# Kernel tuning notes

Measured on AMD Instinct MI355X. Metric: run time of the kernel, lower is better.

The kernel has to match this reference:

```python
import jax, jax.numpy as jnp
import numpy as np


def setup_inputs() -> dict:
    key = jax.random.key(0)
    ks = jax.random.split(key, 7)
    B, S, D, E, R, K = 64, 577, 1024, 8, 16, 2
    x = jax.random.normal(ks[0], (B, S, D), dtype=jnp.float32)
    top_k_indices = jax.random.randint(ks[1], (B, K), 0, E, dtype=jnp.int64)
    # gates are softmax over top-k logits in the original GatingNetwork
    top_k_gates = jax.nn.softmax(jax.random.normal(ks[2], (B, K), dtype=jnp.float32), axis=-1)
    weight_fixed = jax.random.normal(ks[3], (D, D), dtype=jnp.float32) * 0.02
    A_all = jax.random.normal(ks[4], (E, R, D), dtype=jnp.float32) * 0.02
    B_all = jax.random.normal(ks[5], (E, D, R), dtype=jnp.float32) * 0.02
    bias = jax.random.normal(ks[6], (D,), dtype=jnp.float32) * 0.02
    return {"x": x, "top_k_indices": top_k_indices, "top_k_gates": top_k_gates,
            "weight_fixed": weight_fixed, "A_all": A_all, "B_all": B_all, "bias": bias}


def reference(x, top_k_indices, top_k_gates, weight_fixed, A_all, B_all, bias):
    # x: [B,S,D]; top_k_indices/gates: [B,K]; weight_fixed: [O,D]
    # A_all: [E,R,D]; B_all: [E,O,R]; bias: [O]
    output_fixed = jnp.einsum('bsd,od->bso', x, weight_fixed)
    A_sel = A_all[top_k_indices]            # [B,K,R,D] gathered per-batch expert A
    B_sel = B_all[top_k_indices]            # [B,K,O,R]
    x_a = jnp.einsum('bsd,bkrd->bksr', x, A_sel)          # x @ A^T per chosen expert
    expert_out = jnp.einsum('bksr,bkor->bkso', x_a, B_sel)  # (xA^T) @ B^T
    expert_output = jnp.einsum('bkso,bk->bso', expert_out, top_k_gates)
    return output_fixed + expert_output + bias
```

## Files before the change

### kernel.cpp

```cpp
#include <hip/hip_runtime.h>
#include <hip/hip_bf16.h>
#include <stdint.h>

#define M_REAL 36928LL
#define M_PAD  36992LL
#define DDIM   1024
#define SSEQ   577
#define NBATCH 64

typedef __attribute__((ext_vector_type(8))) short bf16x8;
typedef __attribute__((ext_vector_type(4))) float f32x4;

#define XBF_OFF   0ULL
#define WBF_OFF   75759616ULL
#define ABF_OFF   77856768ULL
#define XABF_OFF  78118912ULL
#define GBBF_OFF  80486400ULL
#define WS_NEED   84680704ULL

__device__ __forceinline__ unsigned short f2bf(float f) {
  union { float f; unsigned int u; } v; v.f = f;
  unsigned int u = v.u;
  unsigned int r = (u + 0x7fffu + ((u >> 16) & 1u)) >> 16;
  return (unsigned short)r;
}

__device__ __forceinline__ bf16x8 cvt8(const float* __restrict__ p) {
  float4 a = *(const float4*)p;
  float4 b = *(const float4*)(p + 4);
  bf16x8 o;
  o[0] = (short)f2bf(a.x); o[1] = (short)f2bf(a.y);
  o[2] = (short)f2bf(a.z); o[3] = (short)f2bf(a.w);
  o[4] = (short)f2bf(b.x); o[5] = (short)f2bf(b.y);
  o[6] = (short)f2bf(b.z); o[7] = (short)f2bf(b.w);
  return o;
}

#define GLOAD_LDS16(gsrc, ldst)                                                  \
  __builtin_amdgcn_global_load_lds((const __attribute__((address_space(1))) void*)(gsrc), \
                                   (__attribute__((address_space(3))) void*)(ldst), 16, 0, 0)

__global__ void prep_kernel(const float* __restrict__ W,
                            const float* __restrict__ A_all,
                            const float* __restrict__ B_all,
                            const int* __restrict__ idx,
                            const float* __restrict__ gates,
                            unsigned short* __restrict__ wbf,
                            unsigned short* __restrict__ abf,
                            unsigned short* __restrict__ gbbf,
                            unsigned short* __restrict__ xbf,
                            unsigned short* __restrict__ xabf) {
  const int W_UNITS = 131072;
  const int A_UNITS = 16384;
  const int G_UNITS = 65536;
  const int XP_UNITS = 8192;
  const int P_UNITS = 2048;
  const int TOTAL = W_UNITS + A_UNITS + G_UNITS + XP_UNITS + P_UNITS;
  int u = blockIdx.x * blockDim.x + threadIdx.x;
  int stride = gridDim.x * blockDim.x;
  for (; u < TOTAL; u += stride) {
    if (u < W_UNITS) {
      int i = u * 8;
      *(bf16x8*)(wbf + i) = cvt8(W + i);
    } else if (u < W_UNITS + A_UNITS) {
      int i = (u - W_UNITS) * 8;
      *(bf16x8*)(abf + i) = cvt8(A_all + i);
    } else if (u < W_UNITS + A_UNITS + G_UNITS) {
      int v = u - W_UNITS - A_UNITS;
      int b = v >> 10;
      int n = v & 1023;
      unsigned short tmp[32];
#pragma unroll
      for (int k = 0; k < 2; ++k) {
        int e = idx[b * 2 + k];
        float g = gates[b * 2 + k];
        const float* Br = B_all + ((size_t)e * 1024 + n) * 16;
#pragma unroll
        for (int r = 0; r < 16; ++r) tmp[k * 16 + r] = f2bf(g * Br[r]);
      }
      unsigned short* dst = gbbf + (size_t)v * 32;
#pragma unroll
      for (int j = 0; j < 32; ++j) dst[j] = tmp[j];
    } else if (u < W_UNITS + A_UNITS + G_UNITS + XP_UNITS) {
      int v = u - W_UNITS - A_UNITS - G_UNITS;
      bf16x8 z;
#pragma unroll
      for (int j = 0; j < 8; ++j) z[j] = 0;
      *(bf16x8*)(xbf + (size_t)M_REAL * DDIM + (size_t)v * 8) = z;
    } else {
      int v = u - W_UNITS - A_UNITS - G_UNITS - XP_UNITS;
      xabf[(size_t)M_REAL * 32 + v] = 0;
    }
  }
}

__global__ __launch_bounds__(256) void cast_xa_kernel(
    const float* __restrict__ x,
    const unsigned short* __restrict__ abf,
    const int* __restrict__ idx,
    unsigned short* __restrict__ xbf,
    unsigned short* __restrict__ xabf) {
  int bid = blockIdx.x;
  int b = bid / 10;
  int s0 = (bid % 10) * 64;
  int wave = threadIdx.x >> 6;
  int lane = threadIdx.x & 63;
  int l15 = lane & 15, lhi = lane >> 4;

  int srow = s0 + wave * 16 + l15;
  bool valid = srow < SSEQ;
  long long mrow = (long long)b * SSEQ + (valid ? srow : 0);
  const float* xrow = x + (size_t)mrow * DDIM;
  unsigned short* xbrow = xbf + (size_t)mrow * DDIM;
  int e0 = idx[b * 2 + 0], e1 = idx[b * 2 + 1];
  const unsigned short* ar0 = abf + ((size_t)e0 * 16 + l15) * DDIM;
  const unsigned short* ar1 = abf + ((size_t)e1 * 16 + l15) * DDIM;

  f32x4 acc0 = {0.f, 0.f, 0.f, 0.f}, acc1 = {0.f, 0.f, 0.f, 0.f};
  for (int k = 0; k < DDIM; k += 32) {
    int ko = k + lhi * 8;
    bf16x8 a;
    if (valid) {
      a = cvt8(xrow + ko);
      *(bf16x8*)(xbrow + ko) = a;
    } else {
#pragma unroll
      for (int j = 0; j < 8; ++j) a[j] = 0;
    }
    bf16x8 b0 = *(const bf16x8*)(ar0 + ko);
    bf16x8 b1 = *(const bf16x8*)(ar1 + ko);
    acc0 = __builtin_amdgcn_mfma_f32_16x16x32_bf16(a, b0, acc0, 0, 0, 0);
    acc1 = __builtin_amdgcn_mfma_f32_16x16x32_bf16(a, b1, acc1, 0, 0, 0);
  }
  int sout = s0 + wave * 16 + lhi * 4;
#pragma unroll
  for (int reg = 0; reg < 4; ++reg) {
    int s = sout + reg;
    if (s < SSEQ) {
      size_t mo = ((size_t)b * SSEQ + s) * 32;
      xabf[mo + l15]      = f2bf(acc0[reg]);
      xabf[mo + 16 + l15] = f2bf(acc1[reg]);
    }
  }
}

#define BM 128
#define BN 128
#define BKT 64
__global__ __launch_bounds__(256, 2) void gemm_kernel(
    const unsigned short* __restrict__ xbf,
    const unsigned short* __restrict__ wbf,
    const unsigned short* __restrict__ xabf,
    const unsigned short* __restrict__ gbbf,
    const float* __restrict__ bias,
    float* __restrict__ out) {
  __shared__ unsigned short As0[8192], As1[8192];
  __shared__ unsigned short Bs0[8192], Bs1[8192];

  int g = blockIdx.x;
  int xcd = g & 7, gi = g >> 3;
  int wg = xcd * 289 + gi;
  const int bm = wg >> 3;
  const int bn = wg & 7;
  const long long m0 = (long long)bm * BM;
  const int n0 = bn * BN;

  const int tid = threadIdx.x;
  const int wave = tid >> 6, lane = tid & 63;
  const int l15 = lane & 15, lhi = lane >> 4;
  const int wm = (wave >> 1) * 64, wn = (wave & 1) * 64;

  f32x4 acc[4][4];
#pragma unroll
  for (int i = 0; i < 4; ++i)
#pragma unroll
    for (int j = 0; j < 4; ++j) acc[i][j] = (f32x4){0.f, 0.f, 0.f, 0.f};

  const int rowbase = wave * 32;
  const int rl = lane >> 3;
  const int csrc = (((lane & 7) ^ rl) << 3);

  const int sl0 = ((lhi ^ (l15 & 7)) << 3);
  const int sl1 = sl0 ^ 32;

#define STAGE(t, As_, Bs_)                                                       \
  do { const size_t ko = (size_t)(t) * BKT;                                      \
    _Pragma("unroll")                                                            \
    for (int i = 0; i < 4; ++i) {                                                \
      int r = rowbase + i * 8;                                                   \
      GLOAD_LDS16(xbf + (size_t)(m0 + r + rl) * DDIM + ko + csrc, &As_[r * BKT]);\
    }                                                                            \
    _Pragma("unroll")                                                            \
    for (int i = 0; i < 4; ++i) {                                                \
      int r = rowbase + i * 8;                                                   \
      GLOAD_LDS16(wbf + (size_t)(n0 + r + rl) * DDIM + ko + csrc, &Bs_[r * BKT]);\
    } } while (0)

#define COMPUTE(As_, Bs_)                                                        \
  do { bf16x8 af[4][2], bfv[4][2];                                               \
    _Pragma("unroll")                                                            \
    for (int f = 0; f < 4; ++f) {                                                \
      af[f][0]  = *(const bf16x8*)&As_[(wm + f * 16 + l15) * BKT + sl0];         \
      af[f][1]  = *(const bf16x8*)&As_[(wm + f * 16 + l15) * BKT + sl1];         \
      bfv[f][0] = *(const bf16x8*)&Bs_[(wn + f * 16 + l15) * BKT + sl0];         \
      bfv[f][1] = *(const bf16x8*)&Bs_[(wn + f * 16 + l15) * BKT + sl1];         \
    }                                                                            \
    _Pragma("unroll")                                                            \
    for (int i = 0; i < 4; ++i)                                                  \
      _Pragma("unroll")                                                          \
      for (int j = 0; j < 4; ++j)                                                \
        _Pragma("unroll")                                                        \
        for (int ks = 0; ks < 2; ++ks)                                           \
          acc[i][j] = __builtin_amdgcn_mfma_f32_16x16x32_bf16(                   \
              af[i][ks], bfv[j][ks], acc[i][j], 0, 0, 0);                        \
  } while (0)

#define BAR() do { __builtin_amdgcn_s_barrier(); asm volatile("" ::: "memory"); } while (0)
#define LGKM0() asm volatile("s_waitcnt lgkmcnt(0)" ::: "memory")
#define VM8() asm volatile("s_waitcnt vmcnt(8)" ::: "memory")
#define VM0() asm volatile("s_waitcnt vmcnt(0)" ::: "memory")

  STAGE(0, As0, Bs0);
  STAGE(1, As1, Bs1);
  VM8();
  BAR();

#pragma unroll 1
  for (int i = 0; i < 8; ++i) {
    const int t = 2 * i;
    COMPUTE(As0, Bs0);
    LGKM0(); BAR();
    if (t + 2 < 16) { STAGE(t + 2, As0, Bs0); VM8(); }
    else            { VM0(); }
    BAR();
    COMPUTE(As1, Bs1);
    if (t + 3 < 16) {
      LGKM0(); BAR();
      STAGE(t + 3, As1, Bs1); VM8();
      BAR();
    }
  }
#undef STAGE
#undef COMPUTE

  long long mlast = m0 + BM - 1; if (mlast > M_REAL - 1) mlast = M_REAL - 1;
  int b_lo = (int)(m0 / SSEQ);
  int b_hi = (int)(mlast / SSEQ);
  for (int bs = b_lo; bs <= b_hi; ++bs) {
    bf16x8 af[4], bfv[4];
#pragma unroll
    for (int f = 0; f < 4; ++f) {
      long long m = m0 + wm + f * 16 + l15;
      bf16x8 v = *(const bf16x8*)&xabf[(size_t)m * 32 + lhi * 8];
      if ((int)(m / SSEQ) != bs) {
#pragma unroll
        for (int j = 0; j < 8; ++j) v[j] = 0;
      }
      af[f] = v;
      int n = n0 + wn + f * 16 + l15;
      bfv[f] = *(const bf16x8*)&gbbf[((size_t)bs * 1024 + n) * 32 + lhi * 8];
    }
#pragma unroll
    for (int i = 0; i < 4; ++i)
#pragma unroll
      for (int j = 0; j < 4; ++j)
        acc[i][j] = __builtin_amdgcn_mfma_f32_16x16x32_bf16(af[i], bfv[j], acc[i][j], 0, 0, 0);
  }

  {
    float* lfs = (float*)(wave < 2 ? (void*)As0 : (void*)Bs0);
    const int ebase = (wave & 1) * 1104;
    const long long mrow0 = m0 + wm;
    const int ncol0 = n0 + wn;
#pragma unroll
    for (int i = 0; i < 4; ++i) {
#pragma unroll
      for (int j = 0; j < 4; ++j) {
        float bv = bias[ncol0 + j * 16 + l15];
#pragma unroll
        for (int reg = 0; reg < 4; ++reg)
          lfs[ebase + (lhi * 4 + reg) * 68 + j * 16 + l15] = acc[i][j][reg] + bv;
      }
#pragma unroll
      for (int rr = 0; rr < 4; ++rr) {
        int row = rr * 4 + lhi;
        f32x4 v = *(const f32x4*)&lfs[ebase + row * 68 + l15 * 4];
        long long m = mrow0 + i * 16 + row;
        if (m < M_REAL)
          __builtin_nontemporal_store(v, (f32x4*)&out[m * DDIM + ncol0 + l15 * 4]);
      }
    }
  }
}

extern "C" void kernel_launch(void* const* d_in, const int* in_sizes, int n_in,
                              void* d_out, int out_size, void* d_ws, size_t ws_size,
                              hipStream_t stream) {
  const float* x      = (const float*)d_in[0];
  const int*   idx    = (const int*)d_in[1];
  const float* gates  = (const float*)d_in[2];
  const float* W      = (const float*)d_in[3];
  const float* A_all  = (const float*)d_in[4];
  const float* B_all  = (const float*)d_in[5];
  const float* bias   = (const float*)d_in[6];
  float* out = (float*)d_out;

  char* ws = (char*)d_ws;
  unsigned short* xbf  = (unsigned short*)(ws + XBF_OFF);
  unsigned short* wbf  = (unsigned short*)(ws + WBF_OFF);
  unsigned short* abf  = (unsigned short*)(ws + ABF_OFF);
  unsigned short* xabf = (unsigned short*)(ws + XABF_OFF);
  unsigned short* gbbf = (unsigned short*)(ws + GBBF_OFF);

  prep_kernel<<<dim3(872), dim3(256), 0, stream>>>(W, A_all, B_all, idx, gates,
                                                   wbf, abf, gbbf, xbf, xabf);
  cast_xa_kernel<<<dim3(640), dim3(256), 0, stream>>>(x, abf, idx, xbf, xabf);
  gemm_kernel<<<dim3(2312), dim3(256), 0, stream>>>(xbf, wbf, xabf, gbbf, bias, out);
}
```

Baseline: 153.2 us.

## Load weight operand fragments directly from global into registers, bypassing LDS

Removes the shared-memory staging buffers for the weight tile and has each wave read its B fragments straight from global memory into registers one k-step ahead. The A tile is still double-buffered in LDS, and the wait counts are adjusted to the new load mix. This halves LDS use and removes the B LDS writes and reads. In exchange, B global loads are narrow, strided and duplicated across waves, and their latency is only partly hidden by a single step of prefetch.

Measured after the change: 241.5 us. 1.58x slower.

```diff
diff --git a/kernel.cpp b/kernel.cpp
--- a/kernel.cpp
+++ b/kernel.cpp
@@ -155,7 +155,6 @@
     const float* __restrict__ bias,
     float* __restrict__ out) {
   __shared__ unsigned short As0[8192], As1[8192];
-  __shared__ unsigned short Bs0[8192], Bs1[8192];
 
   int g = blockIdx.x;
   int xcd = g & 7, gi = g >> 3;
@@ -183,27 +182,31 @@
   const int sl0 = ((lhi ^ (l15 & 7)) << 3);
   const int sl1 = sl0 ^ 32;
 
-#define STAGE(t, As_, Bs_)                                                       \
+  const unsigned short* bpB = wbf + (size_t)(n0 + wn + l15) * DDIM + lhi * 8;
+  bf16x8 bfv[4][2];
+
+#define STAGE_A(t, As_)                                                          \
   do { const size_t ko = (size_t)(t) * BKT;                                      \
     _Pragma("unroll")                                                            \
     for (int i = 0; i < 4; ++i) {                                                \
       int r = rowbase + i * 8;                                                   \
       GLOAD_LDS16(xbf + (size_t)(m0 + r + rl) * DDIM + ko + csrc, &As_[r * BKT]);\
-    }                                                                            \
-    _Pragma("unroll")                                                            \
-    for (int i = 0; i < 4; ++i) {                                                \
-      int r = rowbase + i * 8;                                                   \
-      GLOAD_LDS16(wbf + (size_t)(n0 + r + rl) * DDIM + ko + csrc, &Bs_[r * BKT]);\
     } } while (0)
 
-#define COMPUTE(As_, Bs_)                                                        \
-  do { bf16x8 af[4][2], bfv[4][2];                                               \
+#define LOADB(t)                                                                 \
+  do { const size_t ko = (size_t)(t) * BKT;                                      \
     _Pragma("unroll")                                                            \
     for (int f = 0; f < 4; ++f) {                                                \
-      af[f][0]  = *(const bf16x8*)&As_[(wm + f * 16 + l15) * BKT + sl0];         \
-      af[f][1]  = *(const bf16x8*)&As_[(wm + f * 16 + l15) * BKT + sl1];         \
-      bfv[f][0] = *(const bf16x8*)&Bs_[(wn + f * 16 + l15) * BKT + sl0];         \
-      bfv[f][1] = *(const bf16x8*)&Bs_[(wn + f * 16 + l15) * BKT + sl1];         \
+      bfv[f][0] = *(const bf16x8*)(bpB + (size_t)f * 16 * DDIM + ko);            \
+      bfv[f][1] = *(const bf16x8*)(bpB + (size_t)f * 16 * DDIM + ko + 32);       \
+    } } while (0)
+
+#define COMPUTE(As_)                                                             \
+  do { bf16x8 af[4][2];                                                          \
+    _Pragma("unroll")                                                            \
+    for (int f = 0; f < 4; ++f) {                                                \
+      af[f][0] = *(const bf16x8*)&As_[(wm + f * 16 + l15) * BKT + sl0];          \
+      af[f][1] = *(const bf16x8*)&As_[(wm + f * 16 + l15) * BKT + sl1];          \
     }                                                                            \
     _Pragma("unroll")                                                            \
     for (int i = 0; i < 4; ++i)                                                  \
@@ -217,37 +220,41 @@
 
 #define BAR() do { __builtin_amdgcn_s_barrier(); asm volatile("" ::: "memory"); } while (0)
 #define LGKM0() asm volatile("s_waitcnt lgkmcnt(0)" ::: "memory")
-#define VM8() asm volatile("s_waitcnt vmcnt(8)" ::: "memory")
+#define VM4() asm volatile("s_waitcnt vmcnt(4)" ::: "memory")
 #define VM0() asm volatile("s_waitcnt vmcnt(0)" ::: "memory")
 
-  STAGE(0, As0, Bs0);
-  STAGE(1, As1, Bs1);
-  VM8();
+  STAGE_A(0, As0);
+  LOADB(0);
+  STAGE_A(1, As1);
+  VM4();
   BAR();
 
 #pragma unroll 1
   for (int i = 0; i < 8; ++i) {
     const int t = 2 * i;
-    COMPUTE(As0, Bs0);
+    COMPUTE(As0);
     LGKM0(); BAR();
-    if (t + 2 < 16) { STAGE(t + 2, As0, Bs0); VM8(); }
+    LOADB(t + 1);
+    if (t + 2 < 16) { STAGE_A(t + 2, As0); VM4(); }
     else            { VM0(); }
     BAR();
-    COMPUTE(As1, Bs1);
+    COMPUTE(As1);
     if (t + 3 < 16) {
       LGKM0(); BAR();
-      STAGE(t + 3, As1, Bs1); VM8();
+      LOADB(t + 2);
+      STAGE_A(t + 3, As1); VM4();
       BAR();
     }
   }
-#undef STAGE
+#undef STAGE_A
+#undef LOADB
 #undef COMPUTE
 
   long long mlast = m0 + BM - 1; if (mlast > M_REAL - 1) mlast = M_REAL - 1;
   int b_lo = (int)(m0 / SSEQ);
   int b_hi = (int)(mlast / SSEQ);
   for (int bs = b_lo; bs <= b_hi; ++bs) {
-    bf16x8 af[4], bfv[4];
+    bf16x8 af[4], bfw[4];
 #pragma unroll
     for (int f = 0; f < 4; ++f) {
       long long m = m0 + wm + f * 16 + l15;
@@ -258,17 +265,19 @@
       }
       af[f] = v;
       int n = n0 + wn + f * 16 + l15;
-      bfv[f] = *(const bf16x8*)&gbbf[((size_t)bs * 1024 + n) * 32 + lhi * 8];
+      bfw[f] = *(const bf16x8*)&gbbf[((size_t)bs * 1024 + n) * 32 + lhi * 8];
     }
 #pragma unroll
     for (int i = 0; i < 4; ++i)
 #pragma unroll
       for (int j = 0; j < 4; ++j)
-        acc[i][j] = __builtin_amdgcn_mfma_f32_16x16x32_bf16(af[i], bfv[j], acc[i][j], 0, 0, 0);
-  }
+        acc[i][j] = __builtin_amdgcn_mfma_f32_16x16x32_bf16(af[i], bfw[j], acc[i][j], 0, 0, 0);
+  }
+
+  LGKM0(); BAR();
 
   {
-    float* lfs = (float*)(wave < 2 ? (void*)As0 : (void*)Bs0);
+    float* lfs = (float*)(wave < 2 ? (void*)As0 : (void*)As1);
     const int ebase = (wave & 1) * 1104;
     const long long mrow0 = m0 + wm;
     const int ncol0 = n0 + wn;
```
